# Performance work log

Measured on AMD Instinct MI355X. Metric: run time of the kernel, lower is better.

The kernel has to match this reference:

```python
import jax, jax.numpy as jnp
import numpy as np

NUM_CLASSES = 91
BBOX_XFORM_CLIP = float(np.log(1000.0 / 16.0))
WX, WY, WW, WH = 10.0, 10.0, 5.0, 5.0  # torchvision BoxCoder weights
DETECTIONS_PER_IMG = 100


def _decode_boxes(reg, props):
    # reg: [P, 4*C], props: [P, 4] -> [P, C, 4]  (torchvision BoxCoder.decode)
    widths = props[:, 2] - props[:, 0]
    heights = props[:, 3] - props[:, 1]
    ctr_x = props[:, 0] + 0.5 * widths
    ctr_y = props[:, 1] + 0.5 * heights
    r = reg.reshape(reg.shape[0], -1, 4)
    dx = r[..., 0] / WX
    dy = r[..., 1] / WY
    dw = jnp.minimum(r[..., 2] / WW, BBOX_XFORM_CLIP)
    dh = jnp.minimum(r[..., 3] / WH, BBOX_XFORM_CLIP)
    pcx = dx * widths[:, None] + ctr_x[:, None]
    pcy = dy * heights[:, None] + ctr_y[:, None]
    pw = jnp.exp(dw) * widths[:, None]
    ph = jnp.exp(dh) * heights[:, None]
    return jnp.stack([pcx - 0.5 * pw, pcy - 0.5 * ph, pcx + 0.5 * pw, pcy + 0.5 * ph], axis=-1)


def _clip_boxes(boxes, h, w):
    x = jnp.clip(boxes[..., 0::2], 0.0, float(w))
    y = jnp.clip(boxes[..., 1::2], 0.0, float(h))
    return jnp.stack([x[..., 0], y[..., 0], x[..., 1], y[..., 1]], axis=-1)


def setup_inputs() -> dict:
    key = jax.random.key(0)
    k1, k2, k3, k4, k5 = jax.random.split(key, 5)
    B, P, C, FD = 8, 4096, NUM_CLASSES, 1024
    N = B * P
    class_logits = jax.random.normal(k1, (N, C), dtype=jnp.float32)
    box_regression = 0.5 * jax.random.normal(k2, (N, 4 * C), dtype=jnp.float32)
    # valid proposal boxes inside an 800x800 image: x1<x2, y1<y2
    xy = jax.random.uniform(k3, (N, 2), dtype=jnp.float32) * 700.0
    wh = jax.random.uniform(k4, (N, 2), dtype=jnp.float32) * 96.0 + 4.0
    proposals = jnp.concatenate([xy, xy + wh], axis=-1)
    box_features = jax.random.normal(k5, (N, FD), dtype=jnp.float32)
    return {"class_logits": class_logits, "box_regression": box_regression,
            "proposals": proposals, "box_features": box_features,
            "batch_size": B, "image_h": 800, "image_w": 800}


def reference(class_logits, box_regression, proposals, box_features, batch_size, image_h, image_w):
    B = int(batch_size)
    N = class_logits.shape[0]
    P = N // B
    lg = class_logits.reshape(B, P, NUM_CLASSES)
    rg = box_regression.reshape(B, P, 4 * NUM_CLASSES)
    pr = proposals.reshape(B, P, 4)
    ft = box_features.reshape(B, P, -1)

    def per_image(lg_i, rg_i, pr_i, ft_i):
        boxes = _decode_boxes(rg_i, pr_i)            # [P, C, 4]
        scores = jax.nn.softmax(lg_i, axis=-1)       # [P, C]
        boxes = _clip_boxes(boxes, image_h, image_w)
        boxes = boxes[:, 1:].reshape(-1, 4)          # drop background class -> [P*(C-1), 4]
        scores = scores[:, 1:].reshape(-1)
        # batched_nms with iou_threshold=1.0 never suppresses anything (IoU<=1 always),
        # so keep == indices sorted by score descending, truncated to detections_per_img.
        keep = jnp.argsort(-scores)[:DETECTIONS_PER_IMG]
        boxes = boxes / float(image_h)               # source divides by image_shape[0] only
        kept_boxes = boxes[keep]                     # [D, 4]
        feat_idx = keep // (NUM_CLASSES - 1)         # source: keep / (num_classes-1) int div
        kept_feats = ft_i[feat_idx]                  # [D, FD]
        return kept_boxes, kept_feats

    all_boxes, all_features = jax.vmap(per_image)(lg, rg, pr, ft)
    return all_boxes, all_features
```

## Files before the change

kernel.cpp:

```cpp
#include <hip/hip_runtime.h>

#define NCLS 91
#define NFG 90
#define NDET 100
#define FDIM 1024
#define CAP 4096
#define NBUK 4096
#define BBOX_CLIP 4.135166556742356f
#define K1_TPB 256
#define RPB 32
#define K2_TPB 1024

__global__ __launch_bounds__(K1_TPB) void k1_soft(
        const float* __restrict__ logits, float* __restrict__ rowoff,
        unsigned* __restrict__ maxk, int N) {
    int wave = threadIdx.x >> 6, lane = threadIdx.x & 63;
    int rowbase = blockIdx.x * RPB + wave * (RPB / 4);
    for (int it = 0; it < RPB / 4; it++) {
        long long row = rowbase + it;
        if (row >= N) return;
        const float* r = logits + row * NCLS;
        float l1 = r[lane];
        float l2 = (lane < NCLS - 64) ? r[64 + lane] : -INFINITY;
        float mf = fmaxf((lane == 0) ? -INFINITY : l1, l2);
        #pragma unroll
        for (int o = 32; o; o >>= 1) mf = fmaxf(mf, __shfl_xor(mf, o));
        float m = fmaxf(mf, __shfl(l1, 0));
        float e = expf(l1 - m) + ((lane < NCLS - 64) ? expf(l2 - m) : 0.0f);
        #pragma unroll
        for (int o = 32; o; o >>= 1) e += __shfl_xor(e, o);
        float off = m + logf(e);
        unsigned km = __float_as_uint(expf(mf - off));
        if (lane == 0) { rowoff[row] = off; maxk[row] = km; }
    }
}

__device__ __forceinline__ void find_threshold(const unsigned* hist,
                                               unsigned* wsum, unsigned* sh_lb,
                                               int tid, unsigned target) {
    unsigned local[16]; unsigned s = 0, run = 0;
    if (tid < 256) {
        #pragma unroll
        for (int i = 0; i < 16; i++) { local[i] = hist[tid * 16 + i]; s += local[i]; }
        run = s;
        #pragma unroll
        for (int off = 1; off < 64; off <<= 1) {
            unsigned v = __shfl_down(run, off);
            if ((tid & 63) + off < 64) run += v;
        }
        if ((tid & 63) == 0) wsum[tid >> 6] = run;
    }
    __syncthreads();
    if (tid < 256) {
        int w = tid >> 6;
        #pragma unroll
        for (int ww = 0; ww < 4; ww++) if (ww > w) run += wsum[ww];
        unsigned above = run - s;
        #pragma unroll
        for (int i = 15; i >= 0; i--) {
            unsigned prev = above; above += local[i];
            if (above >= target && prev < target)
                *sh_lb = ((unsigned)(tid * 16 + i)) << 20;
        }
    }
    __syncthreads();
}

__global__ __launch_bounds__(K2_TPB) void k2_select(
        const float* __restrict__ logits, const float* __restrict__ reg,
        const float* __restrict__ props,
        const int* __restrict__ pH, const int* __restrict__ pW,
        const float* __restrict__ rowoff, const unsigned* __restrict__ maxk,
        float* __restrict__ outBoxes, unsigned* __restrict__ keepRow, int P) {
    __shared__ unsigned long long cand[CAP];
    __shared__ unsigned long long cbuf[2048];
    __shared__ unsigned hist[NBUK];
    __shared__ unsigned long long win[NDET];
    __shared__ unsigned wsum[4];
    __shared__ unsigned sh_lb, sh_lb2, sh_nhot, sh_ncand, sh_n2;

    const int img = blockIdx.x;
    const int tid = threadIdx.x;
    const unsigned* mk = maxk + (size_t)img * P;
    unsigned* hot = (unsigned*)cbuf;

    if (tid == 0) { sh_nhot = 0; sh_ncand = 0; sh_n2 = 0; sh_lb = 0; sh_lb2 = 0; }
    for (int b = tid; b < NBUK; b += K2_TPB) hist[b] = 0u;
    __syncthreads();

    {
        const int lane = tid & 63;
        for (int r = tid; r < P + (K2_TPB - 1); r += K2_TPB) {
            unsigned b = (r < P) ? (mk[r] >> 20) : 0xFFFFFFFFu;
            bool done = (r >= P);
            while (true) {
                unsigned long long m = __ballot(!done);
                if (!m) break;
                int leader = __ffsll((long long)m) - 1;
                unsigned lb_ = __shfl(b, leader);
                bool mine = (!done && b == lb_);
                unsigned long long grp = __ballot(mine);
                if (lane == leader) atomicAdd(&hist[lb_], (unsigned)__popcll(grp));
                if (mine) done = true;
            }
        }
    }
    __syncthreads();
    find_threshold(hist, wsum, &sh_lb, tid, NDET);
    const unsigned lb = sh_lb;
    const unsigned lbh = lb ? lb - 1 : 0;

    for (int r = tid; r < P; r += K2_TPB)
        if (mk[r] >= lbh) hot[atomicAdd(&sh_nhot, 1u)] = (unsigned)r;
    __syncthreads();
    const int nhot = (int)sh_nhot;

    const int wave = tid >> 6, lane = tid & 63;
    for (int i = wave; i < nhot; i += K2_TPB / 64) {
        int rl = (int)hot[i];
        long long row = (long long)img * P + rl;
        float off = rowoff[row];
        const float* r = logits + row * NCLS;
        float l1 = r[lane];
        float l2 = (lane < NCLS - 64) ? r[64 + lane] : -INFINITY;
        if (lane >= 1) {
            unsigned k = __float_as_uint(expf(l1 - off));
            if (k >= lb) {
                unsigned pos = atomicAdd(&sh_ncand, 1u);
                if (pos < CAP)
                    cand[pos] = ((unsigned long long)k << 32) |
                                (unsigned)(0xFFFFFFFFu - (unsigned)(rl * NFG + lane - 1));
            }
        }
        if (lane < NCLS - 64) {
            unsigned k = __float_as_uint(expf(l2 - off));
            if (k >= lb) {
                unsigned pos = atomicAdd(&sh_ncand, 1u);
                if (pos < CAP)
                    cand[pos] = ((unsigned long long)k << 32) |
                                (unsigned)(0xFFFFFFFFu - (unsigned)(rl * NFG + 63 + lane));
            }
        }
    }
    __syncthreads();
    unsigned cnt = sh_ncand; if (cnt > CAP) cnt = CAP;

    const unsigned long long* pool = cand;
    unsigned pcnt = cnt;

    if (cnt > 128) {
        for (int b = tid; b < NBUK; b += K2_TPB) hist[b] = 0u;
        __syncthreads();
        for (int i = tid; i < (int)cnt; i += K2_TPB)
            atomicAdd(&hist[(unsigned)(cand[i] >> 52)], 1u);
        __syncthreads();
        find_threshold(hist, wsum, &sh_lb2, tid, NDET);
        unsigned lb2 = sh_lb2;
        for (int i = tid; i < (int)cnt; i += K2_TPB) {
            unsigned long long k64 = cand[i];
            if ((unsigned)(k64 >> 32) >= lb2) {
                unsigned pos = atomicAdd(&sh_n2, 1u);
                if (pos < 2048) cbuf[pos] = k64;
            }
        }
        __syncthreads();
        unsigned cnt2 = sh_n2;
        if (cnt2 <= 2048) { pool = cbuf; pcnt = cnt2; }
    }

    for (unsigned i = wave; i < pcnt; i += K2_TPB / 64) {
        unsigned long long me = pool[i];
        unsigned ng = 0;
        for (unsigned j = lane; j < pcnt; j += 64)
            ng += (pool[j] > me) ? 1u : 0u;
        #pragma unroll
        for (int o = 32; o; o >>= 1) ng += __shfl_xor(ng, o);
        if (lane == 0 && ng < NDET) win[ng] = me;
    }
    __syncthreads();

    if (tid < NDET) {
        unsigned long long key = win[tid];
        unsigned e = 0xFFFFFFFFu - (unsigned)(key & 0xFFFFFFFFull);
        int pr = e / NFG, cm = e - pr * NFG, c = cm + 1;
        long long rw = (long long)img * P + pr;
        float x1 = props[rw * 4 + 0], y1 = props[rw * 4 + 1];
        float x2 = props[rw * 4 + 2], y2 = props[rw * 4 + 3];
        float w = x2 - x1, hgt = y2 - y1;
        float cx = x1 + 0.5f * w, cy = y1 + 0.5f * hgt;
        const float* rr = reg + rw * (4 * NCLS) + 4 * c;
        float dx = rr[0] / 10.0f, dy = rr[1] / 10.0f;
        float dw = fminf(rr[2] / 5.0f, BBOX_CLIP);
        float dh = fminf(rr[3] / 5.0f, BBOX_CLIP);
        float pcx = dx * w + cx, pcy = dy * hgt + cy;
        float pw_ = expf(dw) * w, ph_ = expf(dh) * hgt;
        float bx1 = pcx - 0.5f * pw_, by1 = pcy - 0.5f * ph_;
        float bx2 = pcx + 0.5f * pw_, by2 = pcy + 0.5f * ph_;
        float W = (float)(*pW), H = (float)(*pH);
        bx1 = fminf(fmaxf(bx1, 0.0f), W);
        bx2 = fminf(fmaxf(bx2, 0.0f), W);
        by1 = fminf(fmaxf(by1, 0.0f), H);
        by2 = fminf(fmaxf(by2, 0.0f), H);
        int o = (img * NDET + tid) * 4;
        outBoxes[o + 0] = bx1 / H;
        outBoxes[o + 1] = by1 / H;
        outBoxes[o + 2] = bx2 / H;
        outBoxes[o + 3] = by2 / H;
        keepRow[img * NDET + tid] = (unsigned)rw;
    }
}

__global__ __launch_bounds__(256) void k3_feats(
        const float* __restrict__ feats, const unsigned* __restrict__ keepRow,
        float* __restrict__ outF) {
    int det = blockIdx.x;
    long long r = keepRow[det];
    const float4* src = (const float4*)(feats + r * FDIM);
    float4* dst = (float4*)(outF + (long long)det * FDIM);
    dst[threadIdx.x] = src[threadIdx.x];
}

extern "C" void kernel_launch(void* const* d_in, const int* in_sizes, int n_in,
                              void* d_out, int out_size, void* d_ws, size_t ws_size,
                              hipStream_t stream) {
    const float* logits = (const float*)d_in[0];
    const float* reg    = (const float*)d_in[1];
    const float* props  = (const float*)d_in[2];
    const float* feats  = (const float*)d_in[3];
    const int*   pH     = (const int*)d_in[5];
    const int*   pW     = (const int*)d_in[6];

    int N = in_sizes[0] / NCLS;
    int B = out_size / (NDET * (4 + FDIM));
    int P = N / B;

    char* ws = (char*)d_ws;
    float*    rowoff  = (float*)ws;
    unsigned* maxk    = (unsigned*)(rowoff + N);
    unsigned* keepRow = (unsigned*)(maxk + N);

    float* outBoxes = (float*)d_out;
    float* outFeats = outBoxes + (size_t)B * NDET * 4;

    k1_soft<<<(N + RPB - 1) / RPB, K1_TPB, 0, stream>>>(logits, rowoff, maxk, N);
    k2_select<<<B, K2_TPB, 0, stream>>>(logits, reg, props, pH, pW,
                                        rowoff, maxk, outBoxes, keepRow, P);
    k3_feats<<<B * NDET, 256, 0, stream>>>(feats, keepRow, outFeats);
}
```

Measured before the change: 231.6 us.

## Replace shared histogram threshold search with register-held binary search over buckets

Drops the 4096-bucket shared-memory histogram, with its ballot-aggregated atomics and prefix scan, in both selection passes. Instead each thread keeps its bucket keys in registers and a 12-step binary search counts keys at or above a midpoint through wave reductions and two block barriers per step. This removes shared atomics and histogram zeroing but adds about 24 block-wide syncs per pass. It also hardcodes P at most 8192, since each thread loads only 8 rows.

```diff
diff --git a/kernel.cpp b/kernel.cpp
--- a/kernel.cpp
+++ b/kernel.cpp
@@ -5,7 +5,6 @@
 #define NDET 100
 #define FDIM 1024
 #define CAP 4096
-#define NBUK 4096
 #define BBOX_CLIP 4.135166556742356f
 #define K1_TPB 256
 #define RPB 32
@@ -35,35 +34,31 @@
     }
 }
 
-__device__ __forceinline__ void find_threshold(const unsigned* hist,
-                                               unsigned* wsum, unsigned* sh_lb,
+template<int MV>
+__device__ __forceinline__ unsigned bin_thresh(const unsigned (&v)[MV],
+                                               unsigned* rsum, unsigned* sh_cnt,
                                                int tid, unsigned target) {
-    unsigned local[16]; unsigned s = 0, run = 0;
-    if (tid < 256) {
-        #pragma unroll
-        for (int i = 0; i < 16; i++) { local[i] = hist[tid * 16 + i]; s += local[i]; }
-        run = s;
-        #pragma unroll
-        for (int off = 1; off < 64; off <<= 1) {
-            unsigned v = __shfl_down(run, off);
-            if ((tid & 63) + off < 64) run += v;
-        }
-        if ((tid & 63) == 0) wsum[tid >> 6] = run;
-    }
-    __syncthreads();
-    if (tid < 256) {
-        int w = tid >> 6;
-        #pragma unroll
-        for (int ww = 0; ww < 4; ww++) if (ww > w) run += wsum[ww];
-        unsigned above = run - s;
-        #pragma unroll
-        for (int i = 15; i >= 0; i--) {
-            unsigned prev = above; above += local[i];
-            if (above >= target && prev < target)
-                *sh_lb = ((unsigned)(tid * 16 + i)) << 20;
-        }
-    }
-    __syncthreads();
+    const int lane = tid & 63, wave = tid >> 6;
+    int lo = 0, hi = 4095;
+    while (lo < hi) {
+        int mid = (lo + hi + 1) >> 1;
+        unsigned c = 0;
+        #pragma unroll
+        for (int k = 0; k < MV; k++) c += (v[k] >= (unsigned)mid) ? 1u : 0u;
+        #pragma unroll
+        for (int o = 32; o; o >>= 1) c += __shfl_xor(c, o);
+        if (lane == 0) rsum[wave] = c;
+        __syncthreads();
+        if (tid == 0) {
+            unsigned s = 0;
+            #pragma unroll
+            for (int w = 0; w < (K2_TPB >> 6); w++) s += rsum[w];
+            *sh_cnt = s;
+        }
+        __syncthreads();
+        if (*sh_cnt >= target) lo = mid; else hi = mid - 1;
+    }
+    return (unsigned)lo;
 }
 
 __global__ __launch_bounds__(K2_TPB) void k2_select(
@@ -74,40 +69,27 @@
         float* __restrict__ outBoxes, unsigned* __restrict__ keepRow, int P) {
     __shared__ unsigned long long cand[CAP];
     __shared__ unsigned long long cbuf[2048];
-    __shared__ unsigned hist[NBUK];
     __shared__ unsigned long long win[NDET];
-    __shared__ unsigned wsum[4];
-    __shared__ unsigned sh_lb, sh_lb2, sh_nhot, sh_ncand, sh_n2;
+    __shared__ unsigned rsum[K2_TPB >> 6];
+    __shared__ unsigned sh_cnt, sh_nhot, sh_ncand, sh_n2;
 
     const int img = blockIdx.x;
     const int tid = threadIdx.x;
     const unsigned* mk = maxk + (size_t)img * P;
     unsigned* hot = (unsigned*)cbuf;
 
-    if (tid == 0) { sh_nhot = 0; sh_ncand = 0; sh_n2 = 0; sh_lb = 0; sh_lb2 = 0; }
-    for (int b = tid; b < NBUK; b += K2_TPB) hist[b] = 0u;
-    __syncthreads();
-
-    {
-        const int lane = tid & 63;
-        for (int r = tid; r < P + (K2_TPB - 1); r += K2_TPB) {
-            unsigned b = (r < P) ? (mk[r] >> 20) : 0xFFFFFFFFu;
-            bool done = (r >= P);
-            while (true) {
-                unsigned long long m = __ballot(!done);
-                if (!m) break;
-                int leader = __ffsll((long long)m) - 1;
-                unsigned lb_ = __shfl(b, leader);
-                bool mine = (!done && b == lb_);
-                unsigned long long grp = __ballot(mine);
-                if (lane == leader) atomicAdd(&hist[lb_], (unsigned)__popcll(grp));
-                if (mine) done = true;
-            }
-        }
-    }
-    __syncthreads();
-    find_threshold(hist, wsum, &sh_lb, tid, NDET);
-    const unsigned lb = sh_lb;
+    if (tid == 0) { sh_nhot = 0; sh_ncand = 0; sh_n2 = 0; }
+
+    unsigned bk[8];
+    #pragma unroll
+    for (int k = 0; k < 8; k++) {
+        int r = tid + k * K2_TPB;
+        bk[k] = (r < P) ? (mk[r] >> 20) : 0u;
+    }
+    __syncthreads();
+
+    unsigned lbb = bin_thresh<8>(bk, rsum, &sh_cnt, tid, NDET);
+    const unsigned lb = lbb << 20;
     const unsigned lbh = lb ? lb - 1 : 0;
 
     for (int r = tid; r < P; r += K2_TPB)
@@ -149,13 +131,15 @@
     unsigned pcnt = cnt;
 
     if (cnt > 128) {
-        for (int b = tid; b < NBUK; b += K2_TPB) hist[b] = 0u;
-        __syncthreads();
-        for (int i = tid; i < (int)cnt; i += K2_TPB)
-            atomicAdd(&hist[(unsigned)(cand[i] >> 52)], 1u);
-        __syncthreads();
-        find_threshold(hist, wsum, &sh_lb2, tid, NDET);
-        unsigned lb2 = sh_lb2;
+        unsigned ek[4];
+        #pragma unroll
+        for (int k = 0; k < 4; k++) {
+            unsigned i = (unsigned)tid + k * K2_TPB;
+            ek[k] = (i < cnt) ? (unsigned)(cand[i] >> 52) : 0u;
+        }
+        __syncthreads();
+        unsigned b2 = bin_thresh<4>(ek, rsum, &sh_cnt, tid, NDET);
+        unsigned lb2 = b2 << 20;
         for (int i = tid; i < (int)cnt; i += K2_TPB) {
             unsigned long long k64 = cand[i];
             if ((unsigned)(k64 >> 32) >= lb2) {
```

Result: no change. 233.1 us (+0.6%).
